# Kernel tuning notes

Hardware: AMD Instinct MI355X
Metric: run time of the kernel (lower is better)

The kernel has to match this reference:

```python
import jax, jax.numpy as jnp
import numpy as np

B, T, H, D = 2, 2048, 8, 128
HID = H * D          # 1024
K_CONV = 4
EPS = 1e-5


def causal_dwconv(x, w, b):
    # x: [B,T,C], w: [C,K], b: [C]
    # torch Conv1d(groups=C, padding=K-1) followed by [..., :T] == left-padded causal depthwise conv
    K = w.shape[1]
    Tx = x.shape[1]
    xp = jnp.pad(x, ((0, 0), (K - 1, 0), (0, 0)))
    acc = jnp.zeros_like(x)
    for j in range(K):  # tiny fixed loop over kernel taps
        acc = acc + xp[:, j:j + Tx, :] * w[:, j]
    return acc + b


def setup_inputs() -> dict:
    key = jax.random.key(0)
    ks = jax.random.split(key, 16)
    s = 0.02
    inp = {
        'x':   jax.random.normal(ks[0], (B, T, HID), jnp.float32),
        'Wq':  s * jax.random.normal(ks[1], (HID, H * D), jnp.float32),
        'Wk':  s * jax.random.normal(ks[2], (HID, H * D), jnp.float32),
        'Wv':  s * jax.random.normal(ks[3], (HID, H * D), jnp.float32),
        'Wa':  s * jax.random.normal(ks[4], (HID, H * D), jnp.float32),
        'ba':  jnp.zeros((H * D,), jnp.float32),
        'Wb':  s * jax.random.normal(ks[5], (HID, H), jnp.float32),
        'bb':  jnp.zeros((H,), jnp.float32),
        'Wg':  s * jax.random.normal(ks[6], (HID, H * D), jnp.float32),
        'Wo':  s * jax.random.normal(ks[7], (H * D, HID), jnp.float32),
        'cqw': s * jax.random.normal(ks[8], (H * D, K_CONV), jnp.float32),
        'cqb': jnp.zeros((H * D,), jnp.float32),
        'ckw': s * jax.random.normal(ks[9], (H * D, K_CONV), jnp.float32),
        'ckb': jnp.zeros((H * D,), jnp.float32),
        'cvw': s * jax.random.normal(ks[10], (H * D, K_CONV), jnp.float32),
        'cvb': jnp.zeros((H * D,), jnp.float32),
        'ln_g': jnp.ones((D,), jnp.float32),
        'ln_b': jnp.zeros((D,), jnp.float32),
    }
    return inp


def reference(x, Wq, Wk, Wv, Wa, ba, Wb, bb, Wg, Wo,
              cqw, cqb, ckw, ckb, cvw, cvb, ln_g, ln_b):
    Bx, Tx, _ = x.shape
    q = x @ Wq
    k = x @ Wk
    v = x @ Wv
    q = jax.nn.silu(causal_dwconv(q, cqw, cqb))
    k = jax.nn.silu(causal_dwconv(k, ckw, ckb))
    v = jax.nn.silu(causal_dwconv(v, cvw, cvb))
    q = q.reshape(Bx, Tx, H, D)
    k = k.reshape(Bx, Tx, H, D) * (D ** -0.5)   # k scaled by head_dim_qk**-0.5
    v = v.reshape(Bx, Tx, H, D)
    a = jax.nn.sigmoid(x @ Wa + ba).reshape(Bx, Tx, H, D)
    beta = jax.nn.sigmoid(x @ Wb + bb)           # [B,T,H]

    # delta-rule recurrent scan; state S: [B,H,Dv,Dk]
    def step(S, inp):
        q_t, k_t, v_t, a_t, b_t = inp            # [B,H,D] / beta [B,H]
        delta = jnp.einsum('bhvk,bhk->bhv', S, k_t)
        err = delta - v_t
        S = a_t[..., None] * S - (b_t[..., None] * err)[..., None] * k_t[:, :, None, :]
        o_t = jnp.einsum('bhvk,bhk->bhv', S, q_t)
        return S, o_t

    tfirst = lambda z: jnp.moveaxis(z, 1, 0)     # [B,T,...] -> [T,B,...]
    S0 = jnp.zeros((Bx, H, D, D), x.dtype)
    _, o = jax.lax.scan(step, S0, (tfirst(q), tfirst(k), tfirst(v), tfirst(a), tfirst(beta)))
    o = jnp.moveaxis(o, 0, 1)                    # [B,T,H,D]

    # LayerNorm over head_dim_v
    mu = o.mean(-1, keepdims=True)
    var = ((o - mu) ** 2).mean(-1, keepdims=True)
    o = (o - mu) * jax.lax.rsqrt(var + EPS) * ln_g + ln_b

    g = jax.nn.sigmoid(x @ Wg).reshape(Bx, Tx, H, D)
    o = (o * g).reshape(Bx, Tx, H * D)
    return o @ Wo
```

## Files before the change

### kernel.cpp

```cpp
#include <hip/hip_runtime.h>
#include <hip/hip_bf16.h>
#include <cstdint>
#include <cstddef>

#define BATCH 2
#define TLEN  2048
#define NHEAD 8
#define HD    128
#define HIDN  1024
#define MTOT  4096
#define MAT_ELEMS 1048576
#define XELEMS 4194304
#define SCAN_C 32
#define NCH    64
#define SSC  1024.0f
#define ISSC 0.0009765625f

typedef _Float16 f16;
typedef _Float16 f16x2 __attribute__((ext_vector_type(2)));
typedef _Float16 f16x8 __attribute__((ext_vector_type(8)));
typedef float    f32x4 __attribute__((ext_vector_type(4)));

__device__ __forceinline__ float sigmoidf_(float v) { return 1.0f / (1.0f + __expf(-v)); }

__device__ __forceinline__ float fdot2_(f16x2 a, f16x2 b, float c)
{
#if __has_builtin(__builtin_amdgcn_fdot2)
    return __builtin_amdgcn_fdot2(a, b, c, false);
#else
    return fmaf((float)a.x, (float)b.x, fmaf((float)a.y, (float)b.y, c));
#endif
}

__global__ __launch_bounds__(256) void convert_x_kernel(const float* __restrict__ x,
                                                        f16* __restrict__ x16)
{
    int i = (blockIdx.x * 256 + threadIdx.x) * 4;
    float4 v = *(const float4*)(x + i);
    union { f16 h[4]; uint2 u; } pk;
    pk.h[0] = (f16)v.x; pk.h[1] = (f16)v.y; pk.h[2] = (f16)v.z; pk.h[3] = (f16)v.w;
    *(uint2*)(x16 + i) = pk.u;
}

__global__ __launch_bounds__(256) void transpose_convert_kernel(
    const float* __restrict__ Wq, const float* __restrict__ Wk, const float* __restrict__ Wv,
    const float* __restrict__ Wa, const float* __restrict__ Wg, const float* __restrict__ Wo,
    f16* __restrict__ WT)
{
    __shared__ float tile[32][33];
    int mat = blockIdx.z;
    const float* W = (mat == 0) ? Wq : (mat == 1) ? Wk : (mat == 2) ? Wv
                   : (mat == 3) ? Wa : (mat == 4) ? Wg : Wo;
    int k0 = blockIdx.y * 32, n0 = blockIdx.x * 32;
    int tr = threadIdx.x >> 3;
    int tc = (threadIdx.x & 7) * 4;
    float4 vin = *(const float4*)(W + (size_t)(k0 + tr) * HIDN + n0 + tc);
    tile[tr][tc + 0] = vin.x; tile[tr][tc + 1] = vin.y;
    tile[tr][tc + 2] = vin.z; tile[tr][tc + 3] = vin.w;
    __syncthreads();
    f16* dst = WT + (size_t)(mat * HIDN + n0 + tr) * HIDN + k0 + tc;
    union { f16 h[4]; uint2 u; } pk;
    pk.h[0] = (f16)tile[tc + 0][tr]; pk.h[1] = (f16)tile[tc + 1][tr];
    pk.h[2] = (f16)tile[tc + 2][tr]; pk.h[3] = (f16)tile[tc + 3][tr];
    *(uint2*)dst = pk.u;
}

template <int MODE>
__global__ __launch_bounds__(256) void gemm_f16(
    const f16* __restrict__ A, const f16* __restrict__ BT,
    float* __restrict__ out_f32,
    f16* __restrict__ qkv_hat, float* __restrict__ a_buf, f16* __restrict__ g16,
    const float* __restrict__ ba)
{
    __shared__ __align__(16) f16 As[128][40];
    __shared__ __align__(16) f16 Bs[128][40];
    int m0 = blockIdx.y * 128;
    int n0 = blockIdx.x * 128;
    int tid = threadIdx.x;
    int w = tid >> 6, lane = tid & 63;
    int L16 = lane & 15, quad = lane >> 4;
    int wm = (w >> 1) * 64, wn = (w & 1) * 64;

    f32x4 acc[4][4];
#pragma unroll
    for (int i = 0; i < 4; ++i)
#pragma unroll
        for (int j = 0; j < 4; ++j) acc[i][j] = (f32x4){0.f, 0.f, 0.f, 0.f};

    int ldr = tid >> 2;
    int ldc = (tid & 3) * 8;

    for (int k0 = 0; k0 < 1024; k0 += 32) {
        uint4 a0 = *(const uint4*)(A + (size_t)(m0 + ldr) * HIDN + k0 + ldc);
        uint4 a1 = *(const uint4*)(A + (size_t)(m0 + ldr + 64) * HIDN + k0 + ldc);
        uint4 b0 = *(const uint4*)(BT + (size_t)(n0 + ldr) * HIDN + k0 + ldc);
        uint4 b1 = *(const uint4*)(BT + (size_t)(n0 + ldr + 64) * HIDN + k0 + ldc);
        __syncthreads();
        *(uint4*)(&As[ldr][ldc]) = a0;
        *(uint4*)(&As[ldr + 64][ldc]) = a1;
        *(uint4*)(&Bs[ldr][ldc]) = b0;
        *(uint4*)(&Bs[ldr + 64][ldc]) = b1;
        __syncthreads();
        f16x8 af[4], bf[4];
#pragma unroll
        for (int i = 0; i < 4; ++i) {
            af[i] = *(const f16x8*)(&As[wm + i * 16 + L16][quad * 8]);
            bf[i] = *(const f16x8*)(&Bs[wn + i * 16 + L16][quad * 8]);
        }
#pragma unroll
        for (int i = 0; i < 4; ++i)
#pragma unroll
            for (int j = 0; j < 4; ++j)
                acc[i][j] = __builtin_amdgcn_mfma_f32_16x16x32_f16(af[i], bf[j], acc[i][j], 0, 0, 0);
    }

#pragma unroll
    for (int i = 0; i < 4; ++i) {
#pragma unroll
        for (int j = 0; j < 4; ++j) {
            f32x4 c = acc[i][j];
            int mbase = m0 + wm + i * 16 + quad * 4;
            int n = n0 + wn + j * 16 + L16;
            if (MODE == 1) {
#pragma unroll
                for (int r = 0; r < 4; ++r)
                    out_f32[(size_t)(mbase + r) * HIDN + n] = c[r];
            } else {
                int mat = n >> 10;
                int nn = n & 1023;
                if (mat < 3) {
#pragma unroll
                    for (int r = 0; r < 4; ++r)
                        qkv_hat[(size_t)mat * XELEMS + (size_t)(mbase + r) * HIDN + nn] = (f16)c[r];
                } else if (mat == 3) {
                    float bav = ba[nn];
#pragma unroll
                    for (int r = 0; r < 4; ++r)
                        a_buf[(size_t)(mbase + r) * HIDN + nn] = sigmoidf_(c[r] + bav);
                } else {
#pragma unroll
                    for (int r = 0; r < 4; ++r)
                        g16[(size_t)(mbase + r) * HIDN + nn] = (f16)sigmoidf_(c[r]);
                }
            }
        }
    }
}

__global__ __launch_bounds__(256) void beta_kernel(const float* __restrict__ x,
                                                   const float* __restrict__ Wb,
                                                   const float* __restrict__ bb,
                                                   float* __restrict__ beta_buf)
{
    int row = blockIdx.x;
    int h = threadIdx.x >> 5, lane = threadIdx.x & 31;
    const float* xr = x + (size_t)row * HIDN;
    float part = 0.f;
    for (int i = lane; i < HIDN; i += 32)
        part += xr[i] * Wb[i * NHEAD + h];
#pragma unroll
    for (int m = 1; m <= 16; m <<= 1) part += __shfl_xor(part, m);
    if (lane == 0)
        beta_buf[(size_t)row * NHEAD + h] = sigmoidf_(part + bb[h]);
}

__global__ __launch_bounds__(256) void conv_silu_kernel(
    const f16* __restrict__ qkv_hat,
    const float* __restrict__ cqw, const float* __restrict__ cqb,
    const float* __restrict__ ckw, const float* __restrict__ ckb,
    const float* __restrict__ cvw, const float* __restrict__ cvb,
    f16* __restrict__ qkv16)
{
    int z = blockIdx.y;
    int row = blockIdx.x;
    int tloc = row & (TLEN - 1);
    int c4 = threadIdx.x * 4;
    const f16* src = qkv_hat + (size_t)z * XELEMS;
    const float* w  = (z == 0) ? cqw : (z == 1) ? ckw : cvw;
    const float* bi = (z == 0) ? cqb : (z == 1) ? ckb : cvb;

    float xv[4][4];
#pragma unroll
    for (int j = 0; j < 4; ++j) {
        int tt = tloc - 3 + j;
        if (tt >= 0) {
            const f16* p = src + (size_t)(row - 3 + j) * HIDN + c4;
            xv[j][0] = (float)p[0]; xv[j][1] = (float)p[1];
            xv[j][2] = (float)p[2]; xv[j][3] = (float)p[3];
        } else {
            xv[j][0] = xv[j][1] = xv[j][2] = xv[j][3] = 0.f;
        }
    }
    float scale = (z == 1) ? 0.08838834764831845f : 1.0f;
    union { f16 h[4]; uint2 u; } pk;
#pragma unroll
    for (int cc = 0; cc < 4; ++cc) {
        float4 wc = *(const float4*)(w + (size_t)(c4 + cc) * 4);
        float acc = bi[c4 + cc] + wc.x * xv[0][cc] + wc.y * xv[1][cc]
                                 + wc.z * xv[2][cc] + wc.w * xv[3][cc];
        pk.h[cc] = (f16)(acc * sigmoidf_(acc) * scale);
    }
    *(uint2*)(qkv16 + (size_t)z * XELEMS + (size_t)row * HIDN + c4) = pk.u;
}

__global__ __launch_bounds__(64) void gram_kernel(
    const f16* __restrict__ q16, const f16* __restrict__ k16,
    f16* __restrict__ G_g, f16* __restrict__ KQ_g,
    f16* __restrict__ Gx_g, f16* __restrict__ Qx_g, f16* __restrict__ KT_g)
{
    int ch = blockIdx.x;
    int bh = blockIdx.y;
    int b = bh >> 3, h = bh & 7;
    int lane = threadIdx.x;
    int L16 = lane & 15, quad = lane >> 4;
    size_t rowbase = (size_t)(b * TLEN) * HIDN + h * HD;
    int t0 = ch * SCAN_C;
    bool hasNext = (ch + 1 < NCH);

    union ZU { uint4 u; f16x8 v; };
    ZU zz; zz.u = (uint4){0, 0, 0, 0};

    f16x8 kc[2][4], qc[2][4], kn[2][4], qn[2][4];
#pragma unroll
    for (int nt = 0; nt < 2; ++nt)
#pragma unroll
        for (int kk = 0; kk < 4; ++kk) {
            size_t g = rowbase + (size_t)(t0 + nt * 16 + L16) * HIDN + kk * 32 + quad * 8;
            kc[nt][kk] = *(const f16x8*)(k16 + g);
            qc[nt][kk] = *(const f16x8*)(q16 + g);
            if (hasNext) {
                kn[nt][kk] = *(const f16x8*)(k16 + g + (size_t)SCAN_C * HIDN);
                qn[nt][kk] = *(const f16x8*)(q16 + g + (size_t)SCAN_C * HIDN);
            } else {
                kn[nt][kk] = zz.v; qn[nt][kk] = zz.v;
            }
        }

    f32x4 aG[2][2], aKQ[2][2], aGx[2][2], aQx[2][2];
#pragma unroll
    for (int i = 0; i < 2; ++i)
#pragma unroll
        for (int j = 0; j < 2; ++j) {
            aG[i][j] = (f32x4){0, 0, 0, 0}; aKQ[i][j] = (f32x4){0, 0, 0, 0};
            aGx[i][j] = (f32x4){0, 0, 0, 0}; aQx[i][j] = (f32x4){0, 0, 0, 0};
        }
#pragma unroll
    for (int kk = 0; kk < 4; ++kk)
#pragma unroll
        for (int mt = 0; mt < 2; ++mt)
#pragma unroll
            for (int nt = 0; nt < 2; ++nt) {
                aG[mt][nt]  = __builtin_amdgcn_mfma_f32_16x16x32_f16(kc[mt][kk], kc[nt][kk], aG[mt][nt], 0, 0, 0);
                aKQ[mt][nt] = __builtin_amdgcn_mfma_f32_16x16x32_f16(kc[mt][kk], qc[nt][kk], aKQ[mt][nt], 0, 0, 0);
                aGx[mt][nt] = __builtin_amdgcn_mfma_f32_16x16x32_f16(kc[mt][kk], kn[nt][kk], aGx[mt][nt], 0, 0, 0);
                aQx[mt][nt] = __builtin_amdgcn_mfma_f32_16x16x32_f16(kc[mt][kk], qn[nt][kk], aQx[mt][nt], 0, 0, 0);
            }

    size_t gb = ((size_t)bh * NCH + ch) * 1024;
#pragma unroll
    for (int nt = 0; nt < 2; ++nt) {
        int t = nt * 16 + L16;
#pragma unroll
        for (int mt = 0; mt < 2; ++mt) {
            union { f16 e[4]; uint2 u2; } pg, pq, px, py;
#pragma unroll
            for (int r = 0; r < 4; ++r) {
                pg.e[r] = (f16)aG[mt][nt][r];
                pq.e[r] = (f16)aKQ[mt][nt][r];
                px.e[r] = (f16)aGx[mt][nt][r];
                py.e[r] = (f16)aQx[mt][nt][r];
            }
            *(uint2*)(G_g  + gb + t * 32 + mt * 16 + quad * 4) = pg.u2;
            *(uint2*)(KQ_g + gb + t * 32 + mt * 16 + quad * 4) = pq.u2;
            *(uint2*)(Gx_g + gb + t * 32 + mt * 16 + quad * 4) = px.u2;
            *(uint2*)(Qx_g + gb + t * 32 + mt * 16 + quad * 4) = py.u2;
        }
    }
    size_t kb = ((size_t)bh * NCH + ch) * 4096;
#pragma unroll
    for (int nt = 0; nt < 2; ++nt) {
        int t = nt * 16 + L16;
#pragma unroll
        for (int kk = 0; kk < 4; ++kk)
#pragma unroll
            for (int j = 0; j < 8; ++j) {
                int k = kk * 32 + quad * 8 + j;
                KT_g[kb + (size_t)k * 32 + t] = kc[nt][kk][j];
            }
    }
}

__global__ __launch_bounds__(128) void scan2_kernel(
    const f16* __restrict__ q16, const f16* __restrict__ k16, const f16* __restrict__ v16,
    const float* __restrict__ a_buf, const float* __restrict__ beta_buf,
    const f16* __restrict__ G_g, const f16* __restrict__ KQ_g,
    const f16* __restrict__ Gx_g, const f16* __restrict__ Qx_g, const f16* __restrict__ KT_g,
    float* __restrict__ o_buf)
{
    __shared__ __align__(16) float Sp[16 * 132];
    __shared__ __align__(16) f16   Sp16[16 * 136];
    __shared__ __align__(16) f16   KT_lds[128 * 32];
    __shared__ __align__(16) f16   G_lds[2][1024];
    __shared__ __align__(16) f16   Q_lds[2][1024];
    __shared__ __align__(16) f16   Gx_lds[2][1024];
    __shared__ __align__(16) f16   Qx_lds[2][1024];
    __shared__ __align__(16) float skv[2][16 * 34];
    __shared__ __align__(16) float sqv[2][16 * 34];
    __shared__ __align__(16) float avb[2][16 * 68];
    __shared__ __align__(16) float Bts[2][32];
    __shared__ __align__(16) f16   c16s[2][16 * 40];
    __shared__ __align__(16) float PCs[2][16];

    const int tid = threadIdx.x;
    const int wid = tid >> 6;
    const int lane = tid & 63;
    const int L16 = lane & 15, quad = lane >> 4;
    const int vl = lane >> 2, li = lane & 3;
    const int t_av = lane >> 1, halfsel = lane & 1;

    const int bh = blockIdx.x;
    const int b = bh >> 3, h = bh & 7;
    const int v0 = blockIdx.y * 16;
    const size_t rowbase = (size_t)(b * TLEN) * HIDN + h * HD;
    const size_t gmatbase = (size_t)bh * NCH;

    {
        for (int i = tid; i < 16 * 132; i += 128) Sp[i] = 0.f;
        uint32_t* z;
        z = (uint32_t*)Sp16;    for (int i = tid; i < 16 * 136 / 2; i += 128) z[i] = 0u;
        z = (uint32_t*)KT_lds;  for (int i = tid; i < 128 * 32 / 2;  i += 128) z[i] = 0u;
        z = (uint32_t*)G_lds;   for (int i = tid; i < 1024;          i += 128) z[i] = 0u;
        z = (uint32_t*)Q_lds;   for (int i = tid; i < 1024;          i += 128) z[i] = 0u;
        z = (uint32_t*)Gx_lds;  for (int i = tid; i < 1024;          i += 128) z[i] = 0u;
        z = (uint32_t*)Qx_lds;  for (int i = tid; i < 1024;          i += 128) z[i] = 0u;
        z = (uint32_t*)skv;     for (int i = tid; i < 2 * 16 * 34;   i += 128) z[i] = 0u;
        z = (uint32_t*)sqv;     for (int i = tid; i < 2 * 16 * 34;   i += 128) z[i] = 0u;
        z = (uint32_t*)avb;     for (int i = tid; i < 2 * 16 * 68;   i += 128) z[i] = 0u;
        z = (uint32_t*)Bts;     for (int i = tid; i < 2 * 32;        i += 128) z[i] = 0u;
        z = (uint32_t*)c16s;    for (int i = tid; i < 2 * 16 * 40 / 2; i += 128) z[i] = 0u;
        z = (uint32_t*)PCs;     for (int i = tid; i < 2 * 16;        i += 128) z[i] = 0u;
    }
    __syncthreads();

    if (wid == 1) {
        f16x8 kf[2][4], qf[2][4];

        {
            size_t gb0 = gmatbase * 1024;
            *(uint4*)(&G_lds[0][lane * 16])     = *(const uint4*)(G_g  + gb0 + lane * 16);
            *(uint4*)(&G_lds[0][lane * 16 + 8]) = *(const uint4*)(G_g  + gb0 + lane * 16 + 8);
            *(uint4*)(&Q_lds[0][lane * 16])     = *(const uint4*)(KQ_g + gb0 + lane * 16);
            *(uint4*)(&Q_lds[0][lane * 16 + 8]) = *(const uint4*)(KQ_g + gb0 + lane * 16 + 8);
            size_t ga = rowbase + (size_t)t_av * HIDN + v0 + halfsel * 8;
            float4 ar0 = *(const float4*)(a_buf + ga);
            float4 ar1 = *(const float4*)(a_buf + ga + 4);
            uint4  vr  = *(const uint4*)(v16 + ga);
            float betr = beta_buf[((size_t)(b * TLEN) + t_av) * NHEAD + h];
            const f16* vh = (const f16*)&vr;
            const float* aa0 = (const float*)&ar0;
            const float* aa1 = (const float*)&ar1;
#pragma unroll
            for (int e = 0; e < 4; ++e) {
                float2 wv; wv.x = aa0[e]; wv.y = betr * (float)vh[e];
                *(float2*)(&avb[0][(halfsel * 8 + e) * 68 + 2 * t_av]) = wv;
                float2 wu; wu.x = aa1[e]; wu.y = betr * (float)vh[4 + e];
                *(float2*)(&avb[0][(halfsel * 8 + 4 + e) * 68 + 2 * t_av]) = wu;
            }
            if (halfsel == 0) Bts[0][t_av] = betr;
        }
        __syncthreads();

        for (int ch = 0; ch < NCH; ++ch) {
            const int p = ch & 1;
            const int np = p ^ 1;
            const bool haveNext = (ch + 1 < NCH);

            if (ch >= 1 && ch <= NCH - 2) {
                f16x8 ca = *(const f16x8*)(&c16s[np][L16 * 40 + quad * 8]);
                float pc = PCs[np][L16];
#pragma unroll
                for (int kt = 0; kt < 8; ++kt) {
                    f16x8 bu = *(const f16x8*)(&KT_lds[(kt * 16 + L16) * 32 + quad * 8]);
                    f32x4 d = __builtin_amdgcn_mfma_f32_16x16x32_f16(bu, ca, (f32x4){0, 0, 0, 0}, 0, 0, 0);
                    int idx = L16 * 132 + kt * 16 + quad * 4;
                    float4 s = *(const float4*)(&Sp[idx]);
                    s.x = fmaf(pc, s.x, d[0]);
                    s.y = fmaf(pc, s.y, d[1]);
                    s.z = fmaf(pc, s.z, d[2]);
                    s.w = fmaf(pc, s.w, d[3]);
                    *(float4*)(&Sp[idx]) = s;
                    union { f16 e[4]; uint2 u2; } ph;
                    ph.e[0] = (f16)s.x; ph.e[1] = (f16)s.y;
                    ph.e[2] = (f16)s.z; ph.e[3] = (f16)s.w;
                    *(uint2*)(&Sp16[L16 * 136 + kt * 16 + quad * 4]) = ph.u2;
                }
                f32x4 accK[2], accQ[2];
                accK[0] = (f32x4){0, 0, 0, 0}; accK[1] = (f32x4){0, 0, 0, 0};
                accQ[0] = (f32x4){0, 0, 0, 0}; accQ[1] = (f32x4){0, 0, 0, 0};
#pragma unroll
                for (int kk = 0; kk < 4; ++kk) {
                    f16x8 sf = *(const f16x8*)(&Sp16[L16 * 136 + kk * 32 + quad * 8]);
#pragma unroll
                    for (int nt = 0; nt < 2; ++nt) {
                        accK[nt] = __builtin_amdgcn_mfma_f32_16x16x32_f16(sf, kf[nt][kk], accK[nt], 0, 0, 0);
                        accQ[nt] = __builtin_amdgcn_mfma_f32_16x16x32_f16(sf, qf[nt][kk], accQ[nt], 0, 0, 0);
                    }
                }
#pragma unroll
                for (int nt = 0; nt < 2; ++nt) {
                    int t = nt * 16 + L16;
#pragma unroll
                    for (int r = 0; r < 4; ++r) {
                        skv[np][(quad * 4 + r) * 34 + t] = accK[nt][r];
                        sqv[np][(quad * 4 + r) * 34 + t] = accQ[nt][r];
                    }
                }
            }

            if (haveNext) {
                size_t gbn = (gmatbase + ch + 1) * 1024;
                size_t gbc = (gmatbase + ch) * 1024;
                uint4 tg0 = *(const uint4*)(G_g  + gbn + lane * 16);
                uint4 tg1 = *(const uint4*)(G_g  + gbn + lane * 16 + 8);
                uint4 tq0 = *(const uint4*)(KQ_g + gbn + lane * 16);
                uint4 tq1 = *(const uint4*)(KQ_g + gbn + lane * 16 + 8);
                uint4 tx0 = *(const uint4*)(Gx_g + gbc + lane * 16);
                uint4 tx1 = *(const uint4*)(Gx_g + gbc + lane * 16 + 8);
                uint4 ty0 = *(const uint4*)(Qx_g + gbc + lane * 16);
                uint4 ty1 = *(const uint4*)(Qx_g + gbc + lane * 16 + 8);
                *(uint4*)(&G_lds[np][lane * 16])      = tg0;
                *(uint4*)(&G_lds[np][lane * 16 + 8])  = tg1;
                *(uint4*)(&Q_lds[np][lane * 16])      = tq0;
                *(uint4*)(&Q_lds[np][lane * 16 + 8])  = tq1;
                *(uint4*)(&Gx_lds[np][lane * 16])     = tx0;
                *(uint4*)(&Gx_lds[np][lane * 16 + 8]) = tx1;
                *(uint4*)(&Qx_lds[np][lane * 16])     = ty0;
                *(uint4*)(&Qx_lds[np][lane * 16 + 8]) = ty1;
                size_t kb = (gmatbase + ch) * 4096;
#pragma unroll
                for (int i = 0; i < 8; ++i) {
                    uint4 tk = *(const uint4*)(KT_g + kb + lane * 8 + (size_t)i * 512);
                    *(uint4*)(&KT_lds[lane * 8 + i * 512]) = tk;
                }
                int tn = (ch + 1) * SCAN_C;
                size_t ga = rowbase + (size_t)(tn + t_av) * HIDN + v0 + halfsel * 8;
                float4 ar0 = *(const float4*)(a_buf + ga);
                float4 ar1 = *(const float4*)(a_buf + ga + 4);
                uint4  vr  = *(const uint4*)(v16 + ga);
                float betr = beta_buf[((size_t)(b * TLEN) + tn + t_av) * NHEAD + h];
                const f16* vh = (const f16*)&vr;
                const float* aa0 = (const float*)&ar0;
                const float* aa1 = (const float*)&ar1;
#pragma unroll
                for (int e = 0; e < 4; ++e) {
                    float2 wv; wv.x = aa0[e]; wv.y = betr * (float)vh[e];
                    *(float2*)(&avb[np][(halfsel * 8 + e) * 68 + 2 * t_av]) = wv;
                    float2 wu; wu.x = aa1[e]; wu.y = betr * (float)vh[4 + e];
                    *(float2*)(&avb[np][(halfsel * 8 + 4 + e) * 68 + 2 * t_av]) = wu;
                }
                if (halfsel == 0) Bts[np][t_av] = betr;
            }

            if (ch <= NCH - 3) {
                int tp = (ch + 2) * SCAN_C;
#pragma unroll
                for (int nt = 0; nt < 2; ++nt)
#pragma unroll
                    for (int kk = 0; kk < 4; ++kk) {
                        size_t g = rowbase + (size_t)(tp + nt * 16 + L16) * HIDN + kk * 32 + quad * 8;
                        kf[nt][kk] = *(const f16x8*)(k16 + g);
                        qf[nt][kk] = *(const f16x8*)(q16 + g);
                    }
            }
            __syncthreads();
        }
    } else {
        __syncthreads();
        const size_t obase = rowbase + v0 + vl;

        for (int ch = 0; ch < NCH; ++ch) {
            const int p = ch & 1;
            const int np = p ^ 1;
            const int t0 = ch * SCAN_C;

            {
                f16x8 caf = *(const f16x8*)(&c16s[np][L16 * 40 + quad * 8]);
                f32x4 fK[2], fQ[2];
#pragma unroll
                for (int nt = 0; nt < 2; ++nt) {
                    f16x8 bx = *(const f16x8*)(&Gx_lds[p][(nt * 16 + L16) * 32 + quad * 8]);
                    f16x8 by = *(const f16x8*)(&Qx_lds[p][(nt * 16 + L16) * 32 + quad * 8]);
                    fK[nt] = __builtin_amdgcn_mfma_f32_16x16x32_f16(caf, bx, (f32x4){0, 0, 0, 0}, 0, 0, 0);
                    fQ[nt] = __builtin_amdgcn_mfma_f32_16x16x32_f16(caf, by, (f32x4){0, 0, 0, 0}, 0, 0, 0);
                }
#pragma unroll
                for (int r = 0; r < 4; ++r) {
                    int vv = quad * 4 + r;
                    float Pv = PCs[np][vv];
#pragma unroll
                    for (int nt = 0; nt < 2; ++nt) {
                        int t = nt * 16 + L16;
                        skv[p][vv * 34 + t] = fmaf(Pv, skv[p][vv * 34 + t], fK[nt][r]);
                        sqv[p][vv * 34 + t] = fmaf(Pv, sqv[p][vv * 34 + t], fQ[nt][r]);
                    }
                }
            }

            {
                f16x2 c0, c1, c2, c3;
                c0.x = (f16)0.f; c0.y = (f16)0.f; c1 = c0; c2 = c0; c3 = c0;
                float P = 1.f;
                union RowU { uint4 u4; f16x2 h2[4]; };
#pragma unroll
                for (int t = 0; t < SCAN_C; t += 2) {
                    RowU g0u, g1u, h0u, h1u;
                    g0u.u4 = *(const uint4*)(&G_lds[p][t * 32 + li * 8]);
                    g1u.u4 = *(const uint4*)(&G_lds[p][(t + 1) * 32 + li * 8]);
                    h0u.u4 = *(const uint4*)(&Q_lds[p][t * 32 + li * 8]);
                    h1u.u4 = *(const uint4*)(&Q_lds[p][(t + 1) * 32 + li * 8]);
                    float2 skp = *(const float2*)(&skv[p][vl * 34 + t]);
                    float2 sqp = *(const float2*)(&sqv[p][vl * 34 + t]);
                    float4 ab4 = *(const float4*)(&avb[p][vl * 68 + 2 * t]);
                    float2 btp = *(const float2*)(&Bts[p][t]);
                    float kq00 = (float)Q_lds[p][t * 32 + t];
                    f16x2 dq  = *(const f16x2*)(&Q_lds[p][(t + 1) * 32 + t]);
                    float g01 = (float)G_lds[p][(t + 1) * 32 + t];

                    float pG  = fdot2_(c0, g0u.h2[0], fdot2_(c1, g0u.h2[1], 0.f))
                              + fdot2_(c2, g0u.h2[2], fdot2_(c3, g0u.h2[3], 0.f));
                    float pG1 = fdot2_(c0, g1u.h2[0], fdot2_(c1, g1u.h2[1], 0.f))
                              + fdot2_(c2, g1u.h2[2], fdot2_(c3, g1u.h2[3], 0.f));
                    float pO  = fdot2_(c0, h0u.h2[0], fdot2_(c1, h0u.h2[1], 0.f))
                              + fdot2_(c2, h0u.h2[2], fdot2_(c3, h0u.h2[3], 0.f));
                    float pO1 = fdot2_(c0, h1u.h2[0], fdot2_(c1, h1u.h2[1], 0.f))
                              + fdot2_(c2, h1u.h2[2], fdot2_(c3, h1u.h2[3], 0.f));
                    int tmp;
                    tmp = __builtin_amdgcn_update_dpp(0, __float_as_int(pG),  0xB1, 0xF, 0xF, true); pG  += __int_as_float(tmp);
                    tmp = __builtin_amdgcn_update_dpp(0, __float_as_int(pG1), 0xB1, 0xF, 0xF, true); pG1 += __int_as_float(tmp);
                    tmp = __builtin_amdgcn_update_dpp(0, __float_as_int(pO),  0xB1, 0xF, 0xF, true); pO  += __int_as_float(tmp);
                    tmp = __builtin_amdgcn_update_dpp(0, __float_as_int(pO1), 0xB1, 0xF, 0xF, true); pO1 += __int_as_float(tmp);
                    tmp = __builtin_amdgcn_update_dpp(0, __float_as_int(pG),  0x4E, 0xF, 0xF, true); pG  += __int_as_float(tmp);
                    tmp = __builtin_amdgcn_update_dpp(0, __float_as_int(pG1), 0x4E, 0xF, 0xF, true); pG1 += __int_as_float(tmp);
                    tmp = __builtin_amdgcn_update_dpp(0, __float_as_int(pO),  0x4E, 0xF, 0xF, true); pO  += __int_as_float(tmp);
                    tmp = __builtin_amdgcn_update_dpp(0, __float_as_int(pO1), 0x4E, 0xF, 0xF, true); pO1 += __int_as_float(tmp);

                    float a0 = ab4.x, bv0 = ab4.y, a1 = ab4.z, bv1 = ab4.w;
                    float bt0 = btp.x, bt1 = btp.y;
                    float sk0 = skp.x * ISSC, sk1 = skp.y * ISSC;
                    float sq0 = sqp.x * ISSC, sq1 = sqp.y * ISSC;
                    float kq01 = (float)dq.x, kq11 = (float)dq.y;

                    float x0 = fmaf(P, sk0, pG);
                    float u0 = fmaf(-bt0, x0, bv0);
                    float P0 = P * a0;
                    float o0 = fmaf(a0, pO, u0 * kq00);
                    o0 = fmaf(P0, sq0, o0);
                    float accGv = fmaf(a0, pG1, u0 * g01);
                    float x1 = fmaf(P0, sk1, accGv);
                    float u1 = fmaf(-bt1, x1, bv1);
                    float P1 = P0 * a1;
                    float accOv = fmaf(a0, pO1, u0 * kq01);
                    float o1 = fmaf(a1, accOv, u1 * kq11);
                    o1 = fmaf(P1, sq1, o1);

                    float aa = a0 * a1;
                    f16 aah = (f16)aa;
                    f16x2 aa2; aa2.x = aah; aa2.y = aah;
                    c0 *= aa2; c1 *= aa2; c2 *= aa2; c3 *= aa2;
                    if (li == (t >> 3)) {
                        f16x2 un; un.x = (f16)(u0 * a1); un.y = (f16)u1;
                        int sel = (t & 7) >> 1;
                        if (sel == 0) c0 = un; else if (sel == 1) c1 = un;
                        else if (sel == 2) c2 = un; else c3 = un;
                    }
                    P = P1;
                    if (li == 0) {
                        o_buf[obase + (size_t)(t0 + t) * HIDN]     = o0;
                        o_buf[obase + (size_t)(t0 + t + 1) * HIDN] = o1;
                    }
                }
                f16 s16 = (f16)SSC;
                f16x2 ss2; ss2.x = s16; ss2.y = s16;
                union { f16x2 h2[4]; uint4 u4; } pc;
                pc.h2[0] = c0 * ss2; pc.h2[1] = c1 * ss2; pc.h2[2] = c2 * ss2; pc.h2[3] = c3 * ss2;
                *(uint4*)(&c16s[p][vl * 40 + li * 8]) = pc.u4;
                if (li == 0) PCs[p][vl] = P;
            }
            __syncthreads();
        }
    }
}

__global__ __launch_bounds__(256) void ln_gate_kernel(
    const float* __restrict__ o_buf, const f16* __restrict__ g16,
    const float* __restrict__ lng, const float* __restrict__ lnb,
    f16* __restrict__ og16)
{
    int row = blockIdx.x;
    int h = threadIdx.x >> 5, lane = threadIdx.x & 31;
    size_t base = (size_t)row * HIDN + h * HD + lane * 4;
    float4 x = *(const float4*)(o_buf + base);
    float s  = x.x + x.y + x.z + x.w;
    float sq = x.x * x.x + x.y * x.y + x.z * x.z + x.w * x.w;
#pragma unroll
    for (int m = 1; m <= 16; m <<= 1) {
        s  += __shfl_xor(s, m);
        sq += __shfl_xor(sq, m);
    }
    float mu  = s * (1.0f / 128.0f);
    float var = sq * (1.0f / 128.0f) - mu * mu;
    float inv = 1.0f / sqrtf(var + 1e-5f);
    int d = lane * 4;
    const float* xp = (const float*)&x;
    union { f16 h4[4]; uint2 u; } pk;
#pragma unroll
    for (int j = 0; j < 4; ++j) {
        float on = (xp[j] - mu) * inv * lng[d + j] + lnb[d + j];
        pk.h4[j] = (f16)(on * (float)g16[base + j]);
    }
    *(uint2*)(og16 + base) = pk.u;
}

extern "C" void kernel_launch(void* const* d_in, const int* in_sizes, int n_in,
                              void* d_out, int out_size, void* d_ws, size_t ws_size,
                              hipStream_t stream)
{
    (void)in_sizes; (void)n_in; (void)out_size; (void)ws_size;
    const float* x   = (const float*)d_in[0];
    const float* Wq  = (const float*)d_in[1];
    const float* Wk  = (const float*)d_in[2];
    const float* Wv  = (const float*)d_in[3];
    const float* Wa  = (const float*)d_in[4];
    const float* ba  = (const float*)d_in[5];
    const float* Wb  = (const float*)d_in[6];
    const float* bb  = (const float*)d_in[7];
    const float* Wg  = (const float*)d_in[8];
    const float* Wo  = (const float*)d_in[9];
    const float* cqw = (const float*)d_in[10];
    const float* cqb = (const float*)d_in[11];
    const float* ckw = (const float*)d_in[12];
    const float* ckb = (const float*)d_in[13];
    const float* cvw = (const float*)d_in[14];
    const float* cvb = (const float*)d_in[15];
    const float* lng = (const float*)d_in[16];
    const float* lnb = (const float*)d_in[17];
    float* out = (float*)d_out;

    char* ws = (char*)d_ws;
    f16*   x16      = (f16*)(ws + 0);
    f16*   WT       = (f16*)(ws + 8388608);
    f16*   qkvh     = (f16*)(ws + 20971520);
    f16*   qkv16    = (f16*)(ws + 46137344);
    float* a_buf    = (float*)(ws + 96468992);
    f16*   g16      = (f16*)(ws + 113246208);
    float* beta_buf = (float*)(ws + 121634816);
    float* o_buf    = (float*)(ws + 121765888);
    f16*   og16     = (f16*)(ws + 138543104);

    f16* G_g  = qkvh;
    f16* KQ_g = qkvh + 1048576;
    f16* Gx_g = qkvh + 2097152;
    f16* Qx_g = qkvh + 3145728;
    f16* KT_g = qkvh + 4194304;

    convert_x_kernel<<<dim3(4096), dim3(256), 0, stream>>>(x, x16);
    transpose_convert_kernel<<<dim3(32, 32, 6), dim3(256), 0, stream>>>(Wq, Wk, Wv, Wa, Wg, Wo, WT);
    gemm_f16<0><<<dim3(40, 32), dim3(256), 0, stream>>>(x16, WT, nullptr, qkvh, a_buf, g16, ba);
    beta_kernel<<<dim3(4096), dim3(256), 0, stream>>>(x, Wb, bb, beta_buf);
    conv_silu_kernel<<<dim3(4096, 3), dim3(256), 0, stream>>>(qkvh, cqw, cqb, ckw, ckb, cvw, cvb, qkv16);
    gram_kernel<<<dim3(NCH, 16), dim3(64), 0, stream>>>(
        qkv16, qkv16 + XELEMS, G_g, KQ_g, Gx_g, Qx_g, KT_g);
    scan2_kernel<<<dim3(16, 8), dim3(128), 0, stream>>>(
        qkv16, qkv16 + XELEMS, qkv16 + 2 * (size_t)XELEMS, a_buf, beta_buf,
        G_g, KQ_g, Gx_g, Qx_g, KT_g, o_buf);
    ln_gate_kernel<<<dim3(4096), dim3(256), 0, stream>>>(o_buf, g16, lng, lnb, og16);
    gemm_f16<1><<<dim3(8, 32), dim3(256), 0, stream>>>(og16, WT + 5 * (size_t)MAT_ELEMS, out,
                                                       nullptr, nullptr, nullptr, nullptr);
}
```

Before: 572.3 us.

## Use async global-to-LDS loads and double-buffer KT in the scan producer wave

The producer wave in the scan kernel now issues its next-chunk G/Q/Gx/Qx/KT tile loads as direct global-to-LDS transfers before the state-update MFMAs, instead of doing them after. KT is double-buffered in LDS, and the k/q register prefetch uses ping-pong register sets so loads can overlap the update matmuls. The consumer wave gets raised scheduling priority, and launch bounds pin one block per CU. The cost is more LDS and registers. Whether the async LDS writes have completed at the barrier relies on the compiler's wait insertion.

```diff
diff --git a/kernel.cpp b/kernel.cpp
--- a/kernel.cpp
+++ b/kernel.cpp
@@ -30,6 +30,13 @@
 #else
     return fmaf((float)a.x, (float)b.x, fmaf((float)a.y, (float)b.y, c));
 #endif
+}
+
+__device__ __forceinline__ void gload_lds16(const f16* g, f16* l)
+{
+    __builtin_amdgcn_global_load_lds(
+        (const __attribute__((address_space(1))) uint32_t*)(g),
+        (__attribute__((address_space(3))) uint32_t*)(l), 16, 0, 0);
 }
 
 __global__ __launch_bounds__(256) void convert_x_kernel(const float* __restrict__ x,
@@ -290,7 +297,7 @@
     }
 }
 
-__global__ __launch_bounds__(128) void scan2_kernel(
+__global__ __launch_bounds__(128, 1) void scan2_kernel(
     const f16* __restrict__ q16, const f16* __restrict__ k16, const f16* __restrict__ v16,
     const float* __restrict__ a_buf, const float* __restrict__ beta_buf,
     const f16* __restrict__ G_g, const f16* __restrict__ KQ_g,
@@ -299,7 +306,7 @@
 {
     __shared__ __align__(16) float Sp[16 * 132];
     __shared__ __align__(16) f16   Sp16[16 * 136];
-    __shared__ __align__(16) f16   KT_lds[128 * 32];
+    __shared__ __align__(16) f16   KT_lds2[2][4096];
     __shared__ __align__(16) f16   G_lds[2][1024];
     __shared__ __align__(16) f16   Q_lds[2][1024];
     __shared__ __align__(16) f16   Gx_lds[2][1024];
@@ -328,7 +335,7 @@
         for (int i = tid; i < 16 * 132; i += 128) Sp[i] = 0.f;
         uint32_t* z;
         z = (uint32_t*)Sp16;    for (int i = tid; i < 16 * 136 / 2; i += 128) z[i] = 0u;
-        z = (uint32_t*)KT_lds;  for (int i = tid; i < 128 * 32 / 2;  i += 128) z[i] = 0u;
+        z = (uint32_t*)KT_lds2; for (int i = tid; i < 2 * 4096 / 2; i += 128) z[i] = 0u;
         z = (uint32_t*)G_lds;   for (int i = tid; i < 1024;          i += 128) z[i] = 0u;
         z = (uint32_t*)Q_lds;   for (int i = tid; i < 1024;          i += 128) z[i] = 0u;
         z = (uint32_t*)Gx_lds;  for (int i = tid; i < 1024;          i += 128) z[i] = 0u;
@@ -343,7 +350,7 @@
     __syncthreads();
 
     if (wid == 1) {
-        f16x8 kf[2][4], qf[2][4];
+        f16x8 kfA[2][4], qfA[2][4], kfB[2][4], qfB[2][4];
 
         {
             size_t gb0 = gmatbase * 1024;
@@ -370,84 +377,99 @@
         }
         __syncthreads();
 
+#define DO_UPDATE_MM(KF, QF)                                                        \
+        if (ch >= 1 && ch <= NCH - 2) {                                             \
+            f16x8 ca = *(const f16x8*)(&c16s[np][L16 * 40 + quad * 8]);             \
+            float pc = PCs[np][L16];                                                \
+            _Pragma("unroll")                                                       \
+            for (int kt = 0; kt < 8; ++kt) {                                        \
+                f16x8 bu = *(const f16x8*)(&KT_lds2[p][(kt * 16 + L16) * 32 + quad * 8]); \
+                f32x4 d = __builtin_amdgcn_mfma_f32_16x16x32_f16(bu, ca, (f32x4){0, 0, 0, 0}, 0, 0, 0); \
+                int idx = L16 * 132 + kt * 16 + quad * 4;                           \
+                float4 s = *(const float4*)(&Sp[idx]);                              \
+                s.x = fmaf(pc, s.x, d[0]);                                          \
+                s.y = fmaf(pc, s.y, d[1]);                                          \
+                s.z = fmaf(pc, s.z, d[2]);                                          \
+                s.w = fmaf(pc, s.w, d[3]);                                          \
+                *(float4*)(&Sp[idx]) = s;                                           \
+                union { f16 e[4]; uint2 u2; } ph;                                   \
+                ph.e[0] = (f16)s.x; ph.e[1] = (f16)s.y;                             \
+                ph.e[2] = (f16)s.z; ph.e[3] = (f16)s.w;                             \
+                *(uint2*)(&Sp16[L16 * 136 + kt * 16 + quad * 4]) = ph.u2;           \
+            }                                                                       \
+            f32x4 accK[2], accQ[2];                                                 \
+            accK[0] = (f32x4){0, 0, 0, 0}; accK[1] = (f32x4){0, 0, 0, 0};           \
+            accQ[0] = (f32x4){0, 0, 0, 0}; accQ[1] = (f32x4){0, 0, 0, 0};           \
+            _Pragma("unroll")                                                       \
+            for (int kk = 0; kk < 4; ++kk) {                                        \
+                f16x8 sf = *(const f16x8*)(&Sp16[L16 * 136 + kk * 32 + quad * 8]);  \
+                _Pragma("unroll")                                                   \
+                for (int nt = 0; nt < 2; ++nt) {                                    \
+                    accK[nt] = __builtin_amdgcn_mfma_f32_16x16x32_f16(sf, KF[nt][kk], accK[nt], 0, 0, 0); \
+                    accQ[nt] = __builtin_amdgcn_mfma_f32_16x16x32_f16(sf, QF[nt][kk], accQ[nt], 0, 0, 0); \
+                }                                                                   \
+            }                                                                       \
+            _Pragma("unroll")                                                       \
+            for (int nt = 0; nt < 2; ++nt) {                                        \
+                int t = nt * 16 + L16;                                              \
+                _Pragma("unroll")                                                   \
+                for (int r = 0; r < 4; ++r) {                                       \
+                    skv[np][(quad * 4 + r) * 34 + t] = accK[nt][r];                 \
+                    sqv[np][(quad * 4 + r) * 34 + t] = accQ[nt][r];                 \
+                }                                                                   \
+            }                                                                       \
+        }
+
+#define DO_PREFETCH(KF, QF)                                                         \
+        if (ch <= NCH - 3) {                                                        \
+            int tp = (ch + 2) * SCAN_C;                                             \
+            _Pragma("unroll")                                                       \
+            for (int nt = 0; nt < 2; ++nt)                                          \
+                _Pragma("unroll")                                                   \
+                for (int kk = 0; kk < 4; ++kk) {                                    \
+                    size_t g = rowbase + (size_t)(tp + nt * 16 + L16) * HIDN + kk * 32 + quad * 8; \
+                    KF[nt][kk] = *(const f16x8*)(k16 + g);                          \
+                    QF[nt][kk] = *(const f16x8*)(q16 + g);                          \
+                }                                                                   \
+        }
+
         for (int ch = 0; ch < NCH; ++ch) {
             const int p = ch & 1;
             const int np = p ^ 1;
             const bool haveNext = (ch + 1 < NCH);
 
-            if (ch >= 1 && ch <= NCH - 2) {
-                f16x8 ca = *(const f16x8*)(&c16s[np][L16 * 40 + quad * 8]);
-                float pc = PCs[np][L16];
-#pragma unroll
-                for (int kt = 0; kt < 8; ++kt) {
-                    f16x8 bu = *(const f16x8*)(&KT_lds[(kt * 16 + L16) * 32 + quad * 8]);
-                    f32x4 d = __builtin_amdgcn_mfma_f32_16x16x32_f16(bu, ca, (f32x4){0, 0, 0, 0}, 0, 0, 0);
-                    int idx = L16 * 132 + kt * 16 + quad * 4;
-                    float4 s = *(const float4*)(&Sp[idx]);
-                    s.x = fmaf(pc, s.x, d[0]);
-                    s.y = fmaf(pc, s.y, d[1]);
-                    s.z = fmaf(pc, s.z, d[2]);
-                    s.w = fmaf(pc, s.w, d[3]);
-                    *(float4*)(&Sp[idx]) = s;
-                    union { f16 e[4]; uint2 u2; } ph;
-                    ph.e[0] = (f16)s.x; ph.e[1] = (f16)s.y;
-                    ph.e[2] = (f16)s.z; ph.e[3] = (f16)s.w;
-                    *(uint2*)(&Sp16[L16 * 136 + kt * 16 + quad * 4]) = ph.u2;
-                }
-                f32x4 accK[2], accQ[2];
-                accK[0] = (f32x4){0, 0, 0, 0}; accK[1] = (f32x4){0, 0, 0, 0};
-                accQ[0] = (f32x4){0, 0, 0, 0}; accQ[1] = (f32x4){0, 0, 0, 0};
-#pragma unroll
-                for (int kk = 0; kk < 4; ++kk) {
-                    f16x8 sf = *(const f16x8*)(&Sp16[L16 * 136 + kk * 32 + quad * 8]);
-#pragma unroll
-                    for (int nt = 0; nt < 2; ++nt) {
-                        accK[nt] = __builtin_amdgcn_mfma_f32_16x16x32_f16(sf, kf[nt][kk], accK[nt], 0, 0, 0);
-                        accQ[nt] = __builtin_amdgcn_mfma_f32_16x16x32_f16(sf, qf[nt][kk], accQ[nt], 0, 0, 0);
-                    }
-                }
-#pragma unroll
-                for (int nt = 0; nt < 2; ++nt) {
-                    int t = nt * 16 + L16;
-#pragma unroll
-                    for (int r = 0; r < 4; ++r) {
-                        skv[np][(quad * 4 + r) * 34 + t] = accK[nt][r];
-                        sqv[np][(quad * 4 + r) * 34 + t] = accQ[nt][r];
-                    }
-                }
-            }
-
+            float4 ar0, ar1; uint4 vr; float betr = 0.f;
             if (haveNext) {
                 size_t gbn = (gmatbase + ch + 1) * 1024;
                 size_t gbc = (gmatbase + ch) * 1024;
-                uint4 tg0 = *(const uint4*)(G_g  + gbn + lane * 16);
-                uint4 tg1 = *(const uint4*)(G_g  + gbn + lane * 16 + 8);
-                uint4 tq0 = *(const uint4*)(KQ_g + gbn + lane * 16);
-                uint4 tq1 = *(const uint4*)(KQ_g + gbn + lane * 16 + 8);
-                uint4 tx0 = *(const uint4*)(Gx_g + gbc + lane * 16);
-                uint4 tx1 = *(const uint4*)(Gx_g + gbc + lane * 16 + 8);
-                uint4 ty0 = *(const uint4*)(Qx_g + gbc + lane * 16);
-                uint4 ty1 = *(const uint4*)(Qx_g + gbc + lane * 16 + 8);
-                *(uint4*)(&G_lds[np][lane * 16])      = tg0;
-                *(uint4*)(&G_lds[np][lane * 16 + 8])  = tg1;
-                *(uint4*)(&Q_lds[np][lane * 16])      = tq0;
-                *(uint4*)(&Q_lds[np][lane * 16 + 8])  = tq1;
-                *(uint4*)(&Gx_lds[np][lane * 16])     = tx0;
-                *(uint4*)(&Gx_lds[np][lane * 16 + 8]) = tx1;
-                *(uint4*)(&Qx_lds[np][lane * 16])     = ty0;
-                *(uint4*)(&Qx_lds[np][lane * 16 + 8]) = ty1;
-                size_t kb = (gmatbase + ch) * 4096;
-#pragma unroll
-                for (int i = 0; i < 8; ++i) {
-                    uint4 tk = *(const uint4*)(KT_g + kb + lane * 8 + (size_t)i * 512);
-                    *(uint4*)(&KT_lds[lane * 8 + i * 512]) = tk;
-                }
+                const f16* gG = G_g  + gbn + lane * 8;
+                const f16* gQ = KQ_g + gbn + lane * 8;
+                const f16* gX = Gx_g + gbc + lane * 8;
+                const f16* gY = Qx_g + gbc + lane * 8;
+                gload_lds16(gG,       &G_lds[np][0]);
+                gload_lds16(gG + 512, &G_lds[np][512]);
+                gload_lds16(gQ,       &Q_lds[np][0]);
+                gload_lds16(gQ + 512, &Q_lds[np][512]);
+                gload_lds16(gX,       &Gx_lds[np][0]);
+                gload_lds16(gX + 512, &Gx_lds[np][512]);
+                gload_lds16(gY,       &Qx_lds[np][0]);
+                gload_lds16(gY + 512, &Qx_lds[np][512]);
+                const f16* gK = KT_g + (gmatbase + ch) * 4096 + lane * 8;
+#pragma unroll
+                for (int i = 0; i < 8; ++i)
+                    gload_lds16(gK + i * 512, &KT_lds2[np][i * 512]);
                 int tn = (ch + 1) * SCAN_C;
                 size_t ga = rowbase + (size_t)(tn + t_av) * HIDN + v0 + halfsel * 8;
-                float4 ar0 = *(const float4*)(a_buf + ga);
-                float4 ar1 = *(const float4*)(a_buf + ga + 4);
-                uint4  vr  = *(const uint4*)(v16 + ga);
-                float betr = beta_buf[((size_t)(b * TLEN) + tn + t_av) * NHEAD + h];
+                ar0 = *(const float4*)(a_buf + ga);
+                ar1 = *(const float4*)(a_buf + ga + 4);
+                vr  = *(const uint4*)(v16 + ga);
+                betr = beta_buf[((size_t)(b * TLEN) + tn + t_av) * NHEAD + h];
+            }
+
+            if ((ch & 1) == 0) { DO_UPDATE_MM(kfA, qfA) DO_PREFETCH(kfB, qfB) }
+            else               { DO_UPDATE_MM(kfB, qfB) DO_PREFETCH(kfA, qfA) }
+
+            if (haveNext) {
                 const f16* vh = (const f16*)&vr;
                 const float* aa0 = (const float*)&ar0;
                 const float* aa1 = (const float*)&ar1;
@@ -460,21 +482,12 @@
                 }
                 if (halfsel == 0) Bts[np][t_av] = betr;
             }
-
-            if (ch <= NCH - 3) {
-                int tp = (ch + 2) * SCAN_C;
-#pragma unroll
-                for (int nt = 0; nt < 2; ++nt)
-#pragma unroll
-                    for (int kk = 0; kk < 4; ++kk) {
-                        size_t g = rowbase + (size_t)(tp + nt * 16 + L16) * HIDN + kk * 32 + quad * 8;
-                        kf[nt][kk] = *(const f16x8*)(k16 + g);
-                        qf[nt][kk] = *(const f16x8*)(q16 + g);
-                    }
-            }
             __syncthreads();
         }
+#undef DO_UPDATE_MM
+#undef DO_PREFETCH
     } else {
+        __builtin_amdgcn_s_setprio(1);
         __syncthreads();
         const size_t obase = rowbase + v0 + vl;
 
```

Result: no change. 576.0 us (+0.7%).
